# Performance work log

Hardware: AMD Instinct MI355X
Metric: run time of the kernel (lower is better)

The kernel has to match this reference:

```python
import jax, jax.numpy as jnp
import numpy as np

N_INT, N_LANE, N_SENS, N_INJ = 50000, 100000, 50000, 20000
H = 128
L = 3

def setup_inputs() -> dict:
    key = jax.random.key(0)
    ks = jax.random.split(key, 24)
    def edges(k1, k2, n_src, n_tgt, e):
        return jnp.stack([
            jax.random.randint(k1, (e,), 0, n_src),
            jax.random.randint(k2, (e,), 0, n_tgt),
        ]).astype(jnp.int64)
    return {
        "x_int":  jax.random.normal(ks[0], (N_INT, 32), jnp.float32),
        "x_lane": jax.random.normal(ks[1], (N_LANE, 16), jnp.float32),
        "x_sens": jax.random.normal(ks[2], (N_SENS, 8), jnp.float32),
        "x_inj":  jax.random.normal(ks[3], (N_INJ, 8), jnp.float32),
        "edge_spatial":   edges(ks[4], ks[5], N_INT, N_INT, 640000),
        "edge_flow_lane": edges(ks[6], ks[7], N_LANE, N_INT, 640000),
        "edge_flow_sens": edges(ks[8], ks[9], N_SENS, N_INT, 320000),
        "edge_incident":  edges(ks[10], ks[11], N_INJ, N_INT, 160000),
        "W_int":  jax.random.normal(ks[12], (32, H), jnp.float32) * 0.1,
        "b_int":  jax.random.normal(ks[13], (H,), jnp.float32) * 0.1,
        "W_lane": jax.random.normal(ks[14], (16, H), jnp.float32) * 0.1,
        "b_lane": jax.random.normal(ks[15], (H,), jnp.float32) * 0.1,
        "W_sens": jax.random.normal(ks[16], (8, H), jnp.float32) * 0.1,
        "b_sens": jax.random.normal(ks[17], (H,), jnp.float32) * 0.1,
        "W_inj":  jax.random.normal(ks[18], (8, H), jnp.float32) * 0.1,
        "b_inj":  jax.random.normal(ks[19], (H,), jnp.float32) * 0.1,
        "self_W": jax.random.normal(ks[20], (L, H, H), jnp.float32) * 0.05,
        "self_b": jax.random.normal(ks[21], (L, H), jnp.float32) * 0.05,
        "rel_W":  jax.random.normal(ks[22], (L, H, H), jnp.float32) * 0.05,
    }

def _relation(src_feat, edge_index, num_targets, W):
    # gather -> linear (no bias) -> scatter-mean onto int-node targets
    msg = src_feat[edge_index[0]] @ W                      # [E, H]
    s = jax.ops.segment_sum(msg, edge_index[1], num_segments=num_targets)
    cnt = jax.ops.segment_sum(jnp.ones((edge_index.shape[1], 1), msg.dtype),
                              edge_index[1], num_segments=num_targets)
    return s / jnp.clip(cnt, 1.0)

def reference(x_int, x_lane, x_sens, x_inj,
              edge_spatial, edge_flow_lane, edge_flow_sens, edge_incident,
              W_int, b_int, W_lane, b_lane, W_sens, b_sens, W_inj, b_inj,
              self_W, self_b, rel_W):
    h_int = x_int @ W_int + b_int
    h_lane = x_lane @ W_lane + b_lane
    h_sens = x_sens @ W_sens + b_sens
    h_inj = x_inj @ W_inj + b_inj
    n = h_int.shape[0]
    for l in range(self_W.shape[0]):
        W = rel_W[l]
        spatial = _relation(h_int, edge_spatial, n, W)
        flow_l = _relation(h_lane, edge_flow_lane, n, W)
        flow_s = _relation(h_sens, edge_flow_sens, n, W)
        inc = _relation(h_inj, edge_incident, n, W)
        h_int = jax.nn.elu(h_int @ self_W[l] + self_b[l] + spatial + flow_l + flow_s + inc)
    return h_int
```

## Files before the change

kernel.cpp:

```cpp
#include <hip/hip_runtime.h>
#include <hip/hip_bf16.h>
#include <math.h>

#define H 128
#define N_REL 4
#define SB 64

typedef float f32x4 __attribute__((ext_vector_type(4)));
typedef __bf16 bf16x8 __attribute__((ext_vector_type(8)));

__device__ __forceinline__ unsigned short f2bf(float f) {
    return __builtin_bit_cast(unsigned short, (__bf16)f);
}
__device__ __forceinline__ unsigned pack2(float lo, float hi) {
    return (unsigned)f2bf(lo) | ((unsigned)f2bf(hi) << 16);
}
__device__ __forceinline__ void acc2(unsigned u, float& a, float& b) {
    union { unsigned u; float f; } x, y;
    x.u = u << 16; y.u = u & 0xffff0000u;
    a += x.f; b += y.f;
}
__device__ __forceinline__ float bflo(unsigned u) {
    union { unsigned u; float f; } x; x.u = u << 16; return x.f;
}
__device__ __forceinline__ float bfhi(unsigned u) {
    union { unsigned u; float f; } x; x.u = u & 0xffff0000u; return x.f;
}

__global__ __launch_bounds__(256) void k_count_all(
    const int* __restrict__ s0, const int* __restrict__ s1,
    const int* __restrict__ s2, const int* __restrict__ s3,
    int4 E, int4 boff, int* __restrict__ cnt_all, int n)
{
    int b = blockIdx.x;
    const int* src; int Er, rel;
    if (b < boff.y)      { rel = 0; src = s0; Er = E.x; }
    else if (b < boff.z) { rel = 1; src = s1; Er = E.y; b -= boff.y; }
    else if (b < boff.w) { rel = 2; src = s2; Er = E.z; b -= boff.z; }
    else                 { rel = 3; src = s3; Er = E.w; b -= boff.w; }
    int e = b * 256 + threadIdx.x;
    if (e < Er) atomicAdd(&cnt_all[(size_t)rel * n + src[Er + e]], 1);
}

__global__ __launch_bounds__(256) void k_scan1(const int* __restrict__ cnt, int n,
                                               int* __restrict__ partial)
{
    int blk = blockIdx.x;
    int chunk = (n + SB - 1) / SB;
    int lo = blk * chunk, hi = min(lo + chunk, n);
    int s = 0;
    for (int i = lo + threadIdx.x; i < hi; i += 256) s += cnt[i];
    __shared__ int sh[256];
    sh[threadIdx.x] = s; __syncthreads();
    for (int d = 128; d; d >>= 1) {
        if (threadIdx.x < d) sh[threadIdx.x] += sh[threadIdx.x + d];
        __syncthreads();
    }
    if (threadIdx.x == 0) partial[blk] = sh[0];
}

__global__ __launch_bounds__(64) void k_scan2(int* __restrict__ partial,
                                              int* __restrict__ rowptr, int n, int E0)
{
    int lane = threadIdx.x;
    int v = partial[lane];
    int inc = v;
    for (int d = 1; d < 64; d <<= 1) {
        int t = __shfl_up(inc, d);
        if (lane >= d) inc += t;
    }
    partial[lane] = inc - v;
    if (lane == 0) rowptr[n] = E0;
}

__global__ __launch_bounds__(256) void k_scan3(const int* __restrict__ cnt,
                                               const int* __restrict__ partial,
                                               int* __restrict__ rowptr,
                                               int* __restrict__ cursor,
                                               float* __restrict__ recip, int n)
{
    int blk = blockIdx.x;
    int chunk = (n + SB - 1) / SB;
    int lo = blk * chunk, hi = min(lo + chunk, n);
    int per = (chunk + 255) >> 8;
    int tlo = min(lo + threadIdx.x * per, hi);
    int thi = min(tlo + per, hi);
    int s = 0;
    for (int i = tlo; i < thi; ++i) s += cnt[i];
    __shared__ int sh[256];
    sh[threadIdx.x] = s; __syncthreads();
    for (int d = 1; d < 256; d <<= 1) {
        int t = (threadIdx.x >= d) ? sh[threadIdx.x - d] : 0;
        __syncthreads();
        sh[threadIdx.x] += t;
        __syncthreads();
    }
    int run = partial[blk] + sh[threadIdx.x] - s;
    for (int i = tlo; i < thi; ++i) {
        int c = cnt[i];
        rowptr[i] = run;
        cursor[i] = run;
        recip[i] = (c > 0) ? 1.0f / (float)c : 0.0f;
        run += c;
    }
}

__global__ __launch_bounds__(256) void k_recip123(const int* __restrict__ cnt_all,
                                                  float* __restrict__ recip_all, int n)
{
    int i = blockIdx.x * 256 + threadIdx.x;
    if (i >= 3 * n) return;
    int c = cnt_all[n + i];
    recip_all[n + i] = (c > 0) ? 1.0f / (float)c : 0.0f;
}

__global__ __launch_bounds__(256) void k_fill(const int* __restrict__ s0, int E0,
                                              int* __restrict__ cursor, int* __restrict__ col)
{
    int e = blockIdx.x * 256 + threadIdx.x;
    if (e >= E0) return;
    int t = s0[E0 + e];
    int slot = atomicAdd(&cursor[t], 1);
    col[slot] = s0[e];
}

__global__ __launch_bounds__(256) void k_scatx_all(
    const int* __restrict__ s1, const int* __restrict__ s2, const int* __restrict__ s3,
    const float* __restrict__ xL, const float* __restrict__ xS, const float* __restrict__ xI,
    int E1, int E2, int E3, int b1, int b2,
    float* __restrict__ XL, float* __restrict__ XS, float* __restrict__ XI)
{
    int b = blockIdx.x;
    if (b < b1) {
        int e = b * 16 + (threadIdx.x >> 4);
        if (e >= E1) return;
        int d = threadIdx.x & 15;
        int src = s1[e], tgt = s1[E1 + e];
        unsafeAtomicAdd(&XL[(size_t)tgt * 16 + d], xL[(size_t)src * 16 + d]);
    } else if (b < b2) {
        b -= b1;
        int e = b * 32 + (threadIdx.x >> 3);
        if (e >= E2) return;
        int d = threadIdx.x & 7;
        int src = s2[e], tgt = s2[E2 + e];
        unsafeAtomicAdd(&XS[(size_t)tgt * 8 + d], xS[(size_t)src * 8 + d]);
    } else {
        b -= b2;
        int e = b * 32 + (threadIdx.x >> 3);
        if (e >= E3) return;
        int d = threadIdx.x & 7;
        int src = s3[e], tgt = s3[E3 + e];
        unsafeAtomicAdd(&XI[(size_t)tgt * 8 + d], xI[(size_t)src * 8 + d]);
    }
}

__global__ __launch_bounds__(256) void k_encmfma(const float* __restrict__ x,
                                                 const float* __restrict__ W,
                                                 const float* __restrict__ b,
                                                 unsigned short* __restrict__ h, int n)
{
    __shared__ __align__(16) char WB[128 * 80];
    int tid = threadIdx.x;
    {
        int c = tid & 127, khalf = tid >> 7;
        for (int kk = 0; kk < 16; ++kk) {
            int k = khalf * 16 + kk;
            *(unsigned short*)(WB + c * 80 + k * 2) = f2bf(W[(size_t)k * H + c]);
        }
    }
    int lane = tid & 63, wv = tid >> 6;
    int r16 = lane & 15, kgrp = lane >> 4;
    int rowbase = blockIdx.x * 64 + wv * 16;
    int arow = rowbase + r16; if (arow >= n) arow = n - 1;
    const float* xr = x + (size_t)arow * 32 + kgrp * 8;
    float4 xa = *(const float4*)xr, xb = *(const float4*)(xr + 4);
    bf16x8 af;
    af[0] = (__bf16)xa.x; af[1] = (__bf16)xa.y; af[2] = (__bf16)xa.z; af[3] = (__bf16)xa.w;
    af[4] = (__bf16)xb.x; af[5] = (__bf16)xb.y; af[6] = (__bf16)xb.z; af[7] = (__bf16)xb.w;
    __syncthreads();
#pragma unroll
    for (int ct = 0; ct < 8; ++ct) {
        int c = ct * 16 + r16;
        bf16x8 bf = *(const bf16x8*)(WB + c * 80 + kgrp * 16);
        f32x4 acc = { 0.f, 0.f, 0.f, 0.f };
        acc = __builtin_amdgcn_mfma_f32_16x16x32_bf16(af, bf, acc, 0, 0, 0);
        float bb = b[c];
#pragma unroll
        for (int i = 0; i < 4; ++i) {
            int grow = rowbase + kgrp * 4 + i;
            if (grow < n) h[(size_t)grow * H + c] = f2bf(acc[i] + bb);
        }
    }
}

__global__ __launch_bounds__(256) void k_stat(
    const float* __restrict__ XL, const float* __restrict__ XS, const float* __restrict__ XI,
    const float* __restrict__ WL, const float* __restrict__ WSn, const float* __restrict__ WI,
    const float* __restrict__ bL, const float* __restrict__ bS, const float* __restrict__ bI,
    const float* __restrict__ rL, const float* __restrict__ rS, const float* __restrict__ rI,
    unsigned short* __restrict__ statb, int n)
{
    __shared__ float Wc[32][128];
    __shared__ float xs[8][32];
    int t = threadIdx.x;
    for (int i = t; i < 16 * 128; i += 256) Wc[i >> 7][i & 127] = WL[i];
    for (int i = t; i < 8 * 128; i += 256)  Wc[16 + (i >> 7)][i & 127] = WSn[i];
    for (int i = t; i < 8 * 128; i += 256)  Wc[24 + (i >> 7)][i & 127] = WI[i];
    {
        int rr = t >> 5, k = t & 31;
        int rrow = blockIdx.x * 8 + rr; if (rrow >= n) rrow = n - 1;
        float v;
        if (k < 16)      v = XL[(size_t)rrow * 16 + k] * rL[rrow];
        else if (k < 24) v = XS[(size_t)rrow * 8 + (k - 16)] * rS[rrow];
        else             v = XI[(size_t)rrow * 8 + (k - 24)] * rI[rrow];
        xs[rr][k] = v;
    }
    __syncthreads();
    int rl = t >> 5, c4 = (t & 31) << 2;
    int row = blockIdx.x * 8 + rl;
    float a0 = 0.f, a1 = 0.f, a2 = 0.f, a3 = 0.f;
#pragma unroll
    for (int k = 0; k < 32; ++k) {
        float xv = xs[rl][k];
        a0 += xv * Wc[k][c4 + 0]; a1 += xv * Wc[k][c4 + 1];
        a2 += xv * Wc[k][c4 + 2]; a3 += xv * Wc[k][c4 + 3];
    }
    if (row < n) {
        float mL = (rL[row] > 0.f) ? 1.f : 0.f;
        float mS = (rS[row] > 0.f) ? 1.f : 0.f;
        float mI = (rI[row] > 0.f) ? 1.f : 0.f;
        uint2 res;
        res.x = pack2(a0 + mL * bL[c4 + 0] + mS * bS[c4 + 0] + mI * bI[c4 + 0],
                      a1 + mL * bL[c4 + 1] + mS * bS[c4 + 1] + mI * bI[c4 + 1]);
        res.y = pack2(a2 + mL * bL[c4 + 2] + mS * bS[c4 + 2] + mI * bI[c4 + 2],
                      a3 + mL * bL[c4 + 3] + mS * bS[c4 + 3] + mI * bI[c4 + 3]);
        *(uint2*)(statb + (size_t)row * H + c4) = res;
    }
}

__global__ __launch_bounds__(256) void k_spmm(const unsigned short* __restrict__ hsrc,
                                              const int* __restrict__ rowptr,
                                              const int* __restrict__ col,
                                              const float* __restrict__ recip,
                                              const unsigned short* __restrict__ statb,
                                              unsigned short* __restrict__ aggout, int n)
{
    int row = blockIdx.x * 16 + (threadIdx.x >> 4);
    if (row >= n) return;
    int q = (threadIdx.x & 15) << 3;
    int beg = rowptr[row], end = rowptr[row + 1];

    float a0 = 0.f, a1 = 0.f, a2 = 0.f, a3 = 0.f, a4 = 0.f, a5 = 0.f, a6 = 0.f, a7 = 0.f;
    int e = beg;
    for (; e + 4 <= end; e += 4) {
        int s0 = col[e], s1 = col[e + 1], s2 = col[e + 2], s3 = col[e + 3];
        uint4 v0 = *(const uint4*)(hsrc + (size_t)s0 * H + q);
        uint4 v1 = *(const uint4*)(hsrc + (size_t)s1 * H + q);
        uint4 v2 = *(const uint4*)(hsrc + (size_t)s2 * H + q);
        uint4 v3 = *(const uint4*)(hsrc + (size_t)s3 * H + q);
        acc2(v0.x, a0, a1); acc2(v0.y, a2, a3); acc2(v0.z, a4, a5); acc2(v0.w, a6, a7);
        acc2(v1.x, a0, a1); acc2(v1.y, a2, a3); acc2(v1.z, a4, a5); acc2(v1.w, a6, a7);
        acc2(v2.x, a0, a1); acc2(v2.y, a2, a3); acc2(v2.z, a4, a5); acc2(v2.w, a6, a7);
        acc2(v3.x, a0, a1); acc2(v3.y, a2, a3); acc2(v3.z, a4, a5); acc2(v3.w, a6, a7);
    }
    for (; e < end; ++e) {
        uint4 v0 = *(const uint4*)(hsrc + (size_t)col[e] * H + q);
        acc2(v0.x, a0, a1); acc2(v0.y, a2, a3); acc2(v0.z, a4, a5); acc2(v0.w, a6, a7);
    }

    float r = recip[row];
    size_t o = (size_t)row * H + q;
    uint4 sv = *(const uint4*)(statb + o);
    uint4 w;
    w.x = pack2(a0 * r + bflo(sv.x), a1 * r + bfhi(sv.x));
    w.y = pack2(a2 * r + bflo(sv.y), a3 * r + bfhi(sv.y));
    w.z = pack2(a4 * r + bflo(sv.z), a5 * r + bfhi(sv.z));
    w.w = pack2(a6 * r + bflo(sv.w), a7 * r + bfhi(sv.w));
    *(uint4*)(aggout + o) = w;
}

template<int LAST>
__global__ __launch_bounds__(256) void k_layer(const unsigned short* __restrict__ hb,
                                               const unsigned short* __restrict__ aggb,
                                               const float* __restrict__ Ws,
                                               const float* __restrict__ Wr,
                                               const float* __restrict__ bias,
                                               unsigned short* __restrict__ hbout,
                                               float* __restrict__ fout, int n)
{
    __shared__ __align__(16) char BT[128 * 256 * 2];

    int tid = threadIdx.x;
    {
        int c = tid & 127, half = tid >> 7;
        for (int kc = half; kc < 32; kc += 2) {
            int kk0 = kc * 8;
            const float* Wsrc = (kk0 < 128) ? (Ws + (size_t)kk0 * H + c)
                                            : (Wr + (size_t)(kk0 - 128) * H + c);
            bf16x8 pack;
#pragma unroll
            for (int j = 0; j < 8; ++j) pack[j] = (__bf16)Wsrc[(size_t)j * H];
            int woff = c * 512 + ((kc * 16) ^ ((c & 7) << 4));
            *(bf16x8*)(BT + woff) = pack;
        }
    }

    int lane = tid & 63, wv = tid >> 6;
    int r16 = lane & 15, kgrp = lane >> 4;
    int rowbase = blockIdx.x * 64 + wv * 16;
    int arow = rowbase + r16; if (arow >= n) arow = n - 1;

    bf16x8 afrag[8];
#pragma unroll
    for (int ks = 0; ks < 8; ++ks) {
        int k0 = ks * 32 + kgrp * 8;
        const unsigned short* src = (k0 < 128) ? (hb + (size_t)arow * H + k0)
                                               : (aggb + (size_t)arow * H + (k0 - 128));
        afrag[ks] = *(const bf16x8*)src;
    }
    __syncthreads();

#pragma unroll
    for (int ct = 0; ct < 8; ++ct) {
        int c = ct * 16 + r16;
        f32x4 acc = { 0.f, 0.f, 0.f, 0.f };
#pragma unroll
        for (int ks = 0; ks < 8; ++ks) {
            int kbyte = ks * 64 + kgrp * 16;
            int off = c * 512 + (kbyte ^ ((c & 7) << 4));
            bf16x8 bfrag = *(const bf16x8*)(BT + off);
            acc = __builtin_amdgcn_mfma_f32_16x16x32_bf16(afrag[ks], bfrag, acc, 0, 0, 0);
        }
        float bb = bias[c];
#pragma unroll
        for (int i = 0; i < 4; ++i) {
            int grow = rowbase + kgrp * 4 + i;
            if (grow < n) {
                float v = acc[i] + bb;
                v = (v > 0.f) ? v : (expf(v) - 1.f);
                if (LAST) fout[(size_t)grow * H + c] = v;
                else      hbout[(size_t)grow * H + c] = f2bf(v);
            }
        }
    }
}

extern "C" void kernel_launch(void* const* d_in, const int* in_sizes, int n_in,
                              void* d_out, int out_size, void* d_ws, size_t ws_size,
                              hipStream_t stream)
{
    const float* x_int  = (const float*)d_in[0];
    const float* x_lane = (const float*)d_in[1];
    const float* x_sens = (const float*)d_in[2];
    const float* x_inj  = (const float*)d_in[3];
    const int*   e_sp   = (const int*)d_in[4];
    const int*   e_fl   = (const int*)d_in[5];
    const int*   e_fs   = (const int*)d_in[6];
    const int*   e_in   = (const int*)d_in[7];
    const float* W_int  = (const float*)d_in[8];
    const float* b_int  = (const float*)d_in[9];
    const float* W_lane = (const float*)d_in[10];
    const float* b_lane = (const float*)d_in[11];
    const float* W_sens = (const float*)d_in[12];
    const float* b_sens = (const float*)d_in[13];
    const float* W_inj  = (const float*)d_in[14];
    const float* b_inj  = (const float*)d_in[15];
    const float* self_W = (const float*)d_in[16];
    const float* self_b = (const float*)d_in[17];
    const float* rel_W  = (const float*)d_in[18];

    const int n = in_sizes[0] / 32;
    const int E0 = in_sizes[4] / 2, E1 = in_sizes[5] / 2, E2 = in_sizes[6] / 2, E3 = in_sizes[7] / 2;

    float* out = (float*)d_out;

    char* base = (char*)d_ws;
    size_t off = 0;
    auto carve = [&](size_t bytes) { char* p = base + off; off += (bytes + 15) & ~(size_t)15; return p; };
    unsigned short* hb_a  = (unsigned short*)carve((size_t)n * H * 2);
    unsigned short* hb_b  = (unsigned short*)carve((size_t)n * H * 2);
    unsigned short* aggb  = (unsigned short*)carve((size_t)n * H * 2);
    unsigned short* statb = (unsigned short*)carve((size_t)n * H * 2);
    float* ACC   = (float*)carve((size_t)n * 32 * 4);
    float* XL = ACC;
    float* XS = ACC + (size_t)n * 16;
    float* XI = ACC + (size_t)n * 24;
    float* recip = (float*)carve((size_t)N_REL * n * 4);
    int* cnt_all = (int*)carve((size_t)N_REL * n * 4);
    int* rowptr  = (int*)carve((size_t)(n + 1) * 4);
    int* cursor  = (int*)carve((size_t)n * 4);
    int* partial = (int*)carve((size_t)SB * 4);
    int* col0    = (int*)carve((size_t)E0 * 4);

    int B0 = (E0 + 255) / 256, B1 = (E1 + 255) / 256, B2 = (E2 + 255) / 256, B3 = (E3 + 255) / 256;
    int4 E4   = { E0, E1, E2, E3 };
    int4 boff = { 0, B0, B0 + B1, B0 + B1 + B2 };
    hipMemsetAsync(cnt_all, 0, (size_t)N_REL * n * sizeof(int), stream);
    hipMemsetAsync(ACC, 0, (size_t)n * 32 * sizeof(float), stream);
    k_count_all<<<B0 + B1 + B2 + B3, 256, 0, stream>>>(e_sp, e_fl, e_fs, e_in, E4, boff, cnt_all, n);

    k_scan1<<<SB, 256, 0, stream>>>(cnt_all, n, partial);
    k_scan2<<<1, 64, 0, stream>>>(partial, rowptr, n, E0);
    k_scan3<<<SB, 256, 0, stream>>>(cnt_all, partial, rowptr, cursor, recip, n);
    k_recip123<<<(3 * n + 255) / 256, 256, 0, stream>>>(cnt_all, recip, n);
    k_fill<<<B0, 256, 0, stream>>>(e_sp, E0, cursor, col0);

    const float* r0 = recip;
    const float* r1 = recip + (size_t)n;
    const float* r2 = recip + 2 * (size_t)n;
    const float* r3 = recip + 3 * (size_t)n;

    k_encmfma<<<(n + 63) / 64, 256, 0, stream>>>(x_int, W_int, b_int, hb_a, n);

    int SB1 = (E1 + 15) / 16, SB2 = (E2 + 31) / 32, SB3 = (E3 + 31) / 32;
    k_scatx_all<<<SB1 + SB2 + SB3, 256, 0, stream>>>(e_fl, e_fs, e_in, x_lane, x_sens, x_inj,
                                                     E1, E2, E3, SB1, SB1 + SB2, XL, XS, XI);
    k_stat<<<(n + 7) / 8, 256, 0, stream>>>(XL, XS, XI, W_lane, W_sens, W_inj,
                                            b_lane, b_sens, b_inj, r1, r2, r3, statb, n);

    const int spmm_grid = (n + 15) / 16;
    const int layer_grid = (n + 63) / 64;
    unsigned short* cur = hb_a;
    unsigned short* nxt = hb_b;
    for (int l = 0; l < 3; ++l) {
        k_spmm<<<spmm_grid, 256, 0, stream>>>(cur, rowptr, col0, r0, statb, aggb, n);
        const float* Ws = self_W + (size_t)l * H * H;
        const float* Wr = rel_W  + (size_t)l * H * H;
        const float* bb = self_b + (size_t)l * H;
        if (l == 2)
            k_layer<1><<<layer_grid, 256, 0, stream>>>(cur, aggb, Ws, Wr, bb, nullptr, out, n);
        else
            k_layer<0><<<layer_grid, 256, 0, stream>>>(cur, aggb, Ws, Wr, bb, nxt, nullptr, n);
        unsigned short* t = cur; cur = nxt; nxt = t;
    }
}
```

Before: 386.7 us.

## Fold relation counts into scatter pass and build CSR with per-edge sequence numbers

Counts for the three non-spatial relations are now accumulated as float atomics inside the existing feature scatter kernel, so the separate count pass over those edges and the extra reciprocal kernel go away. The spatial CSR build records each edge's atomic return value as a sequence number during counting, so the fill pass becomes a plain indexed write with no second round of atomics and no cursor array. The two memsets become one. In exchange the scatter kernel issues extra atomics, k_stat computes reciprocals inline, and an E0-sized sequence buffer adds memory traffic.

Measured after the change: 371.4 us. 3.9% less time.

```diff
diff --git a/kernel.cpp b/kernel.cpp
--- a/kernel.cpp
+++ b/kernel.cpp
@@ -27,19 +27,12 @@
     union { unsigned u; float f; } x; x.u = u & 0xffff0000u; return x.f;
 }
 
-__global__ __launch_bounds__(256) void k_count_all(
-    const int* __restrict__ s0, const int* __restrict__ s1,
-    const int* __restrict__ s2, const int* __restrict__ s3,
-    int4 E, int4 boff, int* __restrict__ cnt_all, int n)
-{
-    int b = blockIdx.x;
-    const int* src; int Er, rel;
-    if (b < boff.y)      { rel = 0; src = s0; Er = E.x; }
-    else if (b < boff.z) { rel = 1; src = s1; Er = E.y; b -= boff.y; }
-    else if (b < boff.w) { rel = 2; src = s2; Er = E.z; b -= boff.z; }
-    else                 { rel = 3; src = s3; Er = E.w; b -= boff.w; }
-    int e = b * 256 + threadIdx.x;
-    if (e < Er) atomicAdd(&cnt_all[(size_t)rel * n + src[Er + e]], 1);
+__global__ __launch_bounds__(256) void k_count0(const int* __restrict__ s0, int E0,
+                                                int* __restrict__ cnt, int* __restrict__ seq)
+{
+    int e = blockIdx.x * 256 + threadIdx.x;
+    if (e >= E0) return;
+    seq[e] = atomicAdd(&cnt[s0[E0 + e]], 1);
 }
 
 __global__ __launch_bounds__(256) void k_scan1(const int* __restrict__ cnt, int n,
@@ -76,7 +69,6 @@
 __global__ __launch_bounds__(256) void k_scan3(const int* __restrict__ cnt,
                                                const int* __restrict__ partial,
                                                int* __restrict__ rowptr,
-                                               int* __restrict__ cursor,
                                                float* __restrict__ recip, int n)
 {
     int blk = blockIdx.x;
@@ -99,36 +91,28 @@
     for (int i = tlo; i < thi; ++i) {
         int c = cnt[i];
         rowptr[i] = run;
-        cursor[i] = run;
         recip[i] = (c > 0) ? 1.0f / (float)c : 0.0f;
         run += c;
     }
 }
 
-__global__ __launch_bounds__(256) void k_recip123(const int* __restrict__ cnt_all,
-                                                  float* __restrict__ recip_all, int n)
-{
-    int i = blockIdx.x * 256 + threadIdx.x;
-    if (i >= 3 * n) return;
-    int c = cnt_all[n + i];
-    recip_all[n + i] = (c > 0) ? 1.0f / (float)c : 0.0f;
-}
-
-__global__ __launch_bounds__(256) void k_fill(const int* __restrict__ s0, int E0,
-                                              int* __restrict__ cursor, int* __restrict__ col)
+__global__ __launch_bounds__(256) void k_fill_seq(const int* __restrict__ s0, int E0,
+                                                  const int* __restrict__ rowptr,
+                                                  const int* __restrict__ seq,
+                                                  int* __restrict__ col)
 {
     int e = blockIdx.x * 256 + threadIdx.x;
     if (e >= E0) return;
     int t = s0[E0 + e];
-    int slot = atomicAdd(&cursor[t], 1);
-    col[slot] = s0[e];
+    col[rowptr[t] + seq[e]] = s0[e];
 }
 
 __global__ __launch_bounds__(256) void k_scatx_all(
     const int* __restrict__ s1, const int* __restrict__ s2, const int* __restrict__ s3,
     const float* __restrict__ xL, const float* __restrict__ xS, const float* __restrict__ xI,
     int E1, int E2, int E3, int b1, int b2,
-    float* __restrict__ XL, float* __restrict__ XS, float* __restrict__ XI)
+    float* __restrict__ XL, float* __restrict__ XS, float* __restrict__ XI,
+    float* __restrict__ cL, float* __restrict__ cS, float* __restrict__ cI)
 {
     int b = blockIdx.x;
     if (b < b1) {
@@ -137,6 +121,7 @@
         int d = threadIdx.x & 15;
         int src = s1[e], tgt = s1[E1 + e];
         unsafeAtomicAdd(&XL[(size_t)tgt * 16 + d], xL[(size_t)src * 16 + d]);
+        if (d == 0) unsafeAtomicAdd(&cL[tgt], 1.0f);
     } else if (b < b2) {
         b -= b1;
         int e = b * 32 + (threadIdx.x >> 3);
@@ -144,6 +129,7 @@
         int d = threadIdx.x & 7;
         int src = s2[e], tgt = s2[E2 + e];
         unsafeAtomicAdd(&XS[(size_t)tgt * 8 + d], xS[(size_t)src * 8 + d]);
+        if (d == 0) unsafeAtomicAdd(&cS[tgt], 1.0f);
     } else {
         b -= b2;
         int e = b * 32 + (threadIdx.x >> 3);
@@ -151,6 +137,7 @@
         int d = threadIdx.x & 7;
         int src = s3[e], tgt = s3[E3 + e];
         unsafeAtomicAdd(&XI[(size_t)tgt * 8 + d], xI[(size_t)src * 8 + d]);
+        if (d == 0) unsafeAtomicAdd(&cI[tgt], 1.0f);
     }
 }
 
@@ -197,11 +184,12 @@
     const float* __restrict__ XL, const float* __restrict__ XS, const float* __restrict__ XI,
     const float* __restrict__ WL, const float* __restrict__ WSn, const float* __restrict__ WI,
     const float* __restrict__ bL, const float* __restrict__ bS, const float* __restrict__ bI,
-    const float* __restrict__ rL, const float* __restrict__ rS, const float* __restrict__ rI,
+    const float* __restrict__ cLp, const float* __restrict__ cSp, const float* __restrict__ cIp,
     unsigned short* __restrict__ statb, int n)
 {
     __shared__ float Wc[32][128];
     __shared__ float xs[8][32];
+    __shared__ float msk[8][3];
     int t = threadIdx.x;
     for (int i = t; i < 16 * 128; i += 256) Wc[i >> 7][i & 127] = WL[i];
     for (int i = t; i < 8 * 128; i += 256)  Wc[16 + (i >> 7)][i & 127] = WSn[i];
@@ -210,9 +198,22 @@
         int rr = t >> 5, k = t & 31;
         int rrow = blockIdx.x * 8 + rr; if (rrow >= n) rrow = n - 1;
         float v;
-        if (k < 16)      v = XL[(size_t)rrow * 16 + k] * rL[rrow];
-        else if (k < 24) v = XS[(size_t)rrow * 8 + (k - 16)] * rS[rrow];
-        else             v = XI[(size_t)rrow * 8 + (k - 24)] * rI[rrow];
+        if (k < 16) {
+            float c = cLp[rrow];
+            float r = (c > 0.f) ? 1.0f / c : 0.0f;
+            v = XL[(size_t)rrow * 16 + k] * r;
+            if (k == 0) msk[rr][0] = (c > 0.f) ? 1.f : 0.f;
+        } else if (k < 24) {
+            float c = cSp[rrow];
+            float r = (c > 0.f) ? 1.0f / c : 0.0f;
+            v = XS[(size_t)rrow * 8 + (k - 16)] * r;
+            if (k == 16) msk[rr][1] = (c > 0.f) ? 1.f : 0.f;
+        } else {
+            float c = cIp[rrow];
+            float r = (c > 0.f) ? 1.0f / c : 0.0f;
+            v = XI[(size_t)rrow * 8 + (k - 24)] * r;
+            if (k == 24) msk[rr][2] = (c > 0.f) ? 1.f : 0.f;
+        }
         xs[rr][k] = v;
     }
     __syncthreads();
@@ -226,9 +227,7 @@
         a2 += xv * Wc[k][c4 + 2]; a3 += xv * Wc[k][c4 + 3];
     }
     if (row < n) {
-        float mL = (rL[row] > 0.f) ? 1.f : 0.f;
-        float mS = (rS[row] > 0.f) ? 1.f : 0.f;
-        float mI = (rI[row] > 0.f) ? 1.f : 0.f;
+        float mL = msk[rl][0], mS = msk[rl][1], mI = msk[rl][2];
         uint2 res;
         res.x = pack2(a0 + mL * bL[c4 + 0] + mS * bS[c4 + 0] + mI * bI[c4 + 0],
                       a1 + mL * bL[c4 + 1] + mS * bS[c4 + 1] + mI * bI[c4 + 1]);
@@ -381,49 +380,45 @@
     unsigned short* hb_b  = (unsigned short*)carve((size_t)n * H * 2);
     unsigned short* aggb  = (unsigned short*)carve((size_t)n * H * 2);
     unsigned short* statb = (unsigned short*)carve((size_t)n * H * 2);
-    float* ACC   = (float*)carve((size_t)n * 32 * 4);
-    float* XL = ACC;
-    float* XS = ACC + (size_t)n * 16;
-    float* XI = ACC + (size_t)n * 24;
-    float* recip = (float*)carve((size_t)N_REL * n * 4);
-    int* cnt_all = (int*)carve((size_t)N_REL * n * 4);
+    float* ZERO  = (float*)carve((size_t)n * 36 * 4);
+    float* XL   = ZERO;
+    float* XS   = ZERO + (size_t)n * 16;
+    float* XI   = ZERO + (size_t)n * 24;
+    float* CNT1 = ZERO + (size_t)n * 32;
+    float* CNT2 = ZERO + (size_t)n * 33;
+    float* CNT3 = ZERO + (size_t)n * 34;
+    int*   cnt0 = (int*)(ZERO + (size_t)n * 35);
+    float* recip0 = (float*)carve((size_t)n * 4);
     int* rowptr  = (int*)carve((size_t)(n + 1) * 4);
-    int* cursor  = (int*)carve((size_t)n * 4);
     int* partial = (int*)carve((size_t)SB * 4);
+    int* seq     = (int*)carve((size_t)E0 * 4);
     int* col0    = (int*)carve((size_t)E0 * 4);
 
-    int B0 = (E0 + 255) / 256, B1 = (E1 + 255) / 256, B2 = (E2 + 255) / 256, B3 = (E3 + 255) / 256;
-    int4 E4   = { E0, E1, E2, E3 };
-    int4 boff = { 0, B0, B0 + B1, B0 + B1 + B2 };
-    hipMemsetAsync(cnt_all, 0, (size_t)N_REL * n * sizeof(int), stream);
-    hipMemsetAsync(ACC, 0, (size_t)n * 32 * sizeof(float), stream);
-    k_count_all<<<B0 + B1 + B2 + B3, 256, 0, stream>>>(e_sp, e_fl, e_fs, e_in, E4, boff, cnt_all, n);
-
-    k_scan1<<<SB, 256, 0, stream>>>(cnt_all, n, partial);
+    int B0 = (E0 + 255) / 256;
+
+    hipMemsetAsync(ZERO, 0, (size_t)n * 36 * sizeof(float), stream);
+    k_count0<<<B0, 256, 0, stream>>>(e_sp, E0, cnt0, seq);
+
+    k_scan1<<<SB, 256, 0, stream>>>(cnt0, n, partial);
     k_scan2<<<1, 64, 0, stream>>>(partial, rowptr, n, E0);
-    k_scan3<<<SB, 256, 0, stream>>>(cnt_all, partial, rowptr, cursor, recip, n);
-    k_recip123<<<(3 * n + 255) / 256, 256, 0, stream>>>(cnt_all, recip, n);
-    k_fill<<<B0, 256, 0, stream>>>(e_sp, E0, cursor, col0);
-
-    const float* r0 = recip;
-    const float* r1 = recip + (size_t)n;
-    const float* r2 = recip + 2 * (size_t)n;
-    const float* r3 = recip + 3 * (size_t)n;
+    k_scan3<<<SB, 256, 0, stream>>>(cnt0, partial, rowptr, recip0, n);
+    k_fill_seq<<<B0, 256, 0, stream>>>(e_sp, E0, rowptr, seq, col0);
 
     k_encmfma<<<(n + 63) / 64, 256, 0, stream>>>(x_int, W_int, b_int, hb_a, n);
 
     int SB1 = (E1 + 15) / 16, SB2 = (E2 + 31) / 32, SB3 = (E3 + 31) / 32;
     k_scatx_all<<<SB1 + SB2 + SB3, 256, 0, stream>>>(e_fl, e_fs, e_in, x_lane, x_sens, x_inj,
-                                                     E1, E2, E3, SB1, SB1 + SB2, XL, XS, XI);
+                                                     E1, E2, E3, SB1, SB1 + SB2,
+                                                     XL, XS, XI, CNT1, CNT2, CNT3);
     k_stat<<<(n + 7) / 8, 256, 0, stream>>>(XL, XS, XI, W_lane, W_sens, W_inj,
-                                            b_lane, b_sens, b_inj, r1, r2, r3, statb, n);
+                                            b_lane, b_sens, b_inj, CNT1, CNT2, CNT3, statb, n);
 
     const int spmm_grid = (n + 15) / 16;
     const int layer_grid = (n + 63) / 64;
     unsigned short* cur = hb_a;
     unsigned short* nxt = hb_b;
     for (int l = 0; l < 3; ++l) {
-        k_spmm<<<spmm_grid, 256, 0, stream>>>(cur, rowptr, col0, r0, statb, aggb, n);
+        k_spmm<<<spmm_grid, 256, 0, stream>>>(cur, rowptr, col0, recip0, statb, aggb, n);
         const float* Ws = self_W + (size_t)l * H * H;
         const float* Wr = rel_W  + (size_t)l * H * H;
         const float* bb = self_b + (size_t)l * H;
```
